# Kernel tuning notes

Measured on AMD Instinct MI355X. Metric: run time of the kernel, lower is better.

The kernel has to match this reference:

```python
import jax, jax.numpy as jnp
import numpy as np

BLOCK_SIZE = 128


def setup_inputs() -> dict:
    key = jax.random.key(0)
    kq, kk, kv = jax.random.split(key, 3)
    b, t, e = 16, 8192, 256
    Q = jax.random.normal(kq, (b, t, e), dtype=jnp.float32)
    K = jax.random.normal(kk, (b, t, e), dtype=jnp.float32)
    V = jax.random.normal(kv, (b, t, e), dtype=jnp.float32)
    return {"Q": Q, "K": K, "V": V}


def reference(Q, K, V):
    b, t, e = Q.shape
    bs = BLOCK_SIZE
    n = t // bs
    scale = 1.0 / jnp.sqrt(jnp.asarray(e, Q.dtype))
    Qb = Q.reshape(b, n, bs, e)
    Kb = K.reshape(b, n, bs, e)
    Vb = V.reshape(b, n, bs, e)
    # block-diagonal scores: [b, n, bs, bs]
    Z = jnp.einsum('bnqe,bnke->bnqk', Qb, Kb) * scale
    causal = jnp.triu(jnp.ones((bs, bs), dtype=bool), k=1)  # True above diagonal
    Z = jnp.where(causal, -jnp.inf, Z)
    A = jax.nn.softmax(Z, axis=-1)
    out = jnp.einsum('bnqk,bnke->bnqe', A, Vb).reshape(b, t, e)
    A_flat = A.reshape(b, t, bs)  # matches torch view(b, t, block_size)
    return out, A_flat
```

## Files before the change

kernel.cpp:

```cpp
#include <hip/hip_runtime.h>

#define T_  8192
#define E_  256
#define BS_ 128

typedef __attribute__((ext_vector_type(8))) short bf16x8;
typedef __attribute__((ext_vector_type(4))) float f32x4;

__device__ __forceinline__ unsigned short f2bf(float x) {
    unsigned int u = __float_as_uint(x);
    u += 0x7fffu + ((u >> 16) & 1u);
    return (unsigned short)(u >> 16);
}

__device__ __forceinline__ bf16x8 pack8(f32x4 a, f32x4 b) {
    bf16x8 r;
    r[0] = (short)f2bf(a[0]); r[1] = (short)f2bf(a[1]);
    r[2] = (short)f2bf(a[2]); r[3] = (short)f2bf(a[3]);
    r[4] = (short)f2bf(b[0]); r[5] = (short)f2bf(b[1]);
    r[6] = (short)f2bf(b[2]); r[7] = (short)f2bf(b[3]);
    return r;
}

__global__ __launch_bounds__(256, 2) void dba_qk_softmax(
        const float* __restrict__ Qg, const float* __restrict__ Kg,
        float* __restrict__ Ag)
{
    __shared__ unsigned short Ks[BS_ * E_];

    const int tid  = threadIdx.x;
    const int lane = tid & 63;
    const int w    = tid >> 6;
    const int cl   = lane & 15;
    const int g    = lane >> 4;
    const int bi   = blockIdx.x >> 6;
    const int ni   = blockIdx.x & 63;
    const int base  = (bi * T_ + ni * BS_) * E_;
    const int abase = (bi * T_ + ni * BS_) * BS_;

    {
        const int kq   = (tid & 63) * 4;
        const int nhi  = tid >> 6;
        const int chnk = kq >> 3;
        const int klow = kq & 7;
        #pragma unroll 8
        for (int i = 0; i < 32; ++i) {
            const int n = i * 4 + nhi;
            f32x4 kv = *(const f32x4*)(Kg + base + n * E_ + kq);
            const int chunkp = chnk ^ (n & 15);
            uint2 pk;
            pk.x = (unsigned)f2bf(kv[0]) | ((unsigned)f2bf(kv[1]) << 16);
            pk.y = (unsigned)f2bf(kv[2]) | ((unsigned)f2bf(kv[3]) << 16);
            *(uint2*)&Ks[n * E_ + chunkp * 8 + klow] = pk;
        }
    }
    __syncthreads();

    f32x4 acc[2][8];
    #pragma unroll
    for (int rt = 0; rt < 2; ++rt)
        #pragma unroll
        for (int nt = 0; nt < 8; ++nt)
            acc[rt][nt] = (f32x4){0.f, 0.f, 0.f, 0.f};

    const float* q0p = Qg + base + (w * 32 + cl) * E_;
    const float* q1p = q0p + 16 * E_;
    f32x4 q00 = *(const f32x4*)(q0p + g * 8);
    f32x4 q01 = *(const f32x4*)(q0p + g * 8 + 4);
    f32x4 q10 = *(const f32x4*)(q1p + g * 8);
    f32x4 q11 = *(const f32x4*)(q1p + g * 8 + 4);

    for (int ks = 0; ks < 8; ++ks) {
        bf16x8 aq0 = pack8(q00, q01);
        bf16x8 aq1 = pack8(q10, q11);
        if (ks < 7) {
            const int kn = (ks + 1) * 32 + g * 8;
            q00 = *(const f32x4*)(q0p + kn);
            q01 = *(const f32x4*)(q0p + kn + 4);
            q10 = *(const f32x4*)(q1p + kn);
            q11 = *(const f32x4*)(q1p + kn + 4);
        }
        const int chunkp = (ks * 4 + g) ^ cl;
        #pragma unroll
        for (int nt = 0; nt < 8; ++nt) {
            const int n = nt * 16 + cl;
            bf16x8 bk = *(const bf16x8*)&Ks[n * E_ + chunkp * 8];
            acc[0][nt] = __builtin_amdgcn_mfma_f32_16x16x32_bf16(aq0, bk, acc[0][nt], 0, 0, 0);
            acc[1][nt] = __builtin_amdgcn_mfma_f32_16x16x32_bf16(aq1, bk, acc[1][nt], 0, 0, 0);
        }
    }

    const float scale = 0.0625f;
    const float L2E   = 1.4426950408889634f;
    #pragma unroll
    for (int rt = 0; rt < 2; ++rt) {
        #pragma unroll
        for (int r = 0; r < 4; ++r) {
            const int q = w * 32 + rt * 16 + g * 4 + r;
            float m = -__builtin_inff();
            #pragma unroll
            for (int nt = 0; nt < 8; ++nt) {
                const int c = nt * 16 + cl;
                float z = acc[rt][nt][r] * scale;
                z = (c > q) ? -__builtin_inff() : z;
                acc[rt][nt][r] = z;
                m = fmaxf(m, z);
            }
            m = fmaxf(m, __shfl_xor(m, 1));
            m = fmaxf(m, __shfl_xor(m, 2));
            m = fmaxf(m, __shfl_xor(m, 4));
            m = fmaxf(m, __shfl_xor(m, 8));
            float s = 0.f;
            #pragma unroll
            for (int nt = 0; nt < 8; ++nt) {
                const float p = exp2f((acc[rt][nt][r] - m) * L2E);
                acc[rt][nt][r] = p;
                s += p;
            }
            s += __shfl_xor(s, 1);
            s += __shfl_xor(s, 2);
            s += __shfl_xor(s, 4);
            s += __shfl_xor(s, 8);
            const float rinv = __builtin_amdgcn_rcpf(s);
            #pragma unroll
            for (int nt = 0; nt < 8; ++nt)
                acc[rt][nt][r] *= rinv;
        }
    }

    #pragma unroll
    for (int rt = 0; rt < 2; ++rt)
        #pragma unroll
        for (int nt = 0; nt < 8; ++nt)
            #pragma unroll
            for (int r = 0; r < 4; ++r)
                Ag[abase + (w * 32 + rt * 16 + g * 4 + r) * BS_ + nt * 16 + cl] = acc[rt][nt][r];
}

__global__ __launch_bounds__(256, 2) void dba_av(
        const float* __restrict__ Ag, const float* __restrict__ Vg,
        float* __restrict__ Og)
{
    __shared__ unsigned short Vs[E_ * BS_];

    const int tid  = threadIdx.x;
    const int lane = tid & 63;
    const int w    = tid >> 6;
    const int cl   = lane & 15;
    const int g    = lane >> 4;
    const int bi   = blockIdx.x >> 6;
    const int ni   = blockIdx.x & 63;
    const int base  = (bi * T_ + ni * BS_) * E_;
    const int abase = (bi * T_ + ni * BS_) * BS_;

    {
        const int n  = tid;
        const int nx = n & 15;
        #pragma unroll 8
        for (int i = 0; i < 32; ++i) {
            const int k = i * 4;
            const float* vp = Vg + base + k * E_ + n;
            const float v0 = vp[0];
            const float v1 = vp[E_];
            const float v2 = vp[2 * E_];
            const float v3 = vp[3 * E_];
            const int chunkp = (k >> 3) ^ nx;
            uint2 pk;
            pk.x = (unsigned)f2bf(v0) | ((unsigned)f2bf(v1) << 16);
            pk.y = (unsigned)f2bf(v2) | ((unsigned)f2bf(v3) << 16);
            *(uint2*)&Vs[n * BS_ + chunkp * 8 + (k & 7)] = pk;
        }
    }
    __syncthreads();

    f32x4 acc[2][16];
    #pragma unroll
    for (int rt = 0; rt < 2; ++rt)
        #pragma unroll
        for (int nt = 0; nt < 16; ++nt)
            acc[rt][nt] = (f32x4){0.f, 0.f, 0.f, 0.f};

    const float* a0p = Ag + abase + (w * 32 + cl) * BS_;
    const float* a1p = a0p + 16 * BS_;
    f32x4 a00 = *(const f32x4*)(a0p + g * 8);
    f32x4 a01 = *(const f32x4*)(a0p + g * 8 + 4);
    f32x4 a10 = *(const f32x4*)(a1p + g * 8);
    f32x4 a11 = *(const f32x4*)(a1p + g * 8 + 4);

    for (int ks = 0; ks < 4; ++ks) {
        bf16x8 fa0 = pack8(a00, a01);
        bf16x8 fa1 = pack8(a10, a11);
        if (ks < 3) {
            const int kn = (ks + 1) * 32 + g * 8;
            a00 = *(const f32x4*)(a0p + kn);
            a01 = *(const f32x4*)(a0p + kn + 4);
            a10 = *(const f32x4*)(a1p + kn);
            a11 = *(const f32x4*)(a1p + kn + 4);
        }
        const int chunkp = (ks * 4 + g) ^ cl;
        #pragma unroll
        for (int nt = 0; nt < 16; ++nt) {
            const int nn = nt * 16 + cl;
            bf16x8 bv = *(const bf16x8*)&Vs[nn * BS_ + chunkp * 8];
            acc[0][nt] = __builtin_amdgcn_mfma_f32_16x16x32_bf16(fa0, bv, acc[0][nt], 0, 0, 0);
            acc[1][nt] = __builtin_amdgcn_mfma_f32_16x16x32_bf16(fa1, bv, acc[1][nt], 0, 0, 0);
        }
    }

    #pragma unroll
    for (int rt = 0; rt < 2; ++rt)
        #pragma unroll
        for (int nt = 0; nt < 16; ++nt)
            #pragma unroll
            for (int r = 0; r < 4; ++r)
                Og[base + (w * 32 + rt * 16 + g * 4 + r) * E_ + nt * 16 + cl] = acc[rt][nt][r];
}

extern "C" void kernel_launch(void* const* d_in, const int* in_sizes, int n_in,
                              void* d_out, int out_size, void* d_ws, size_t ws_size,
                              hipStream_t stream) {
    const float* Q = (const float*)d_in[0];
    const float* K = (const float*)d_in[1];
    const float* V = (const float*)d_in[2];
    float* O = (float*)d_out;
    const int b = in_sizes[0] / (T_ * E_);
    float* A = O + (size_t)b * T_ * E_;
    dim3 grid(b * (T_ / BS_));
    dim3 block(256);
    dba_qk_softmax<<<grid, block, 0, stream>>>(Q, K, A);
    dba_av<<<grid, block, 0, stream>>>(A, V, O);
}
```

Before: 474.9 us.

## Fuse QK-softmax and AV into one kernel reusing shared memory

Merges the two kernels into a single 512-thread kernel. Each block first stages K in shared memory and computes the softmaxed scores, writes A to global, then reloads V into the same shared buffer and reads its own A rows back to compute the output. Each wave now handles 16 query rows instead of 32, and Q/K/V loads and O stores use nontemporal hints. The intent is to drop the second launch and let the A read-back come from cache instead of HBM. The cost is an extra block barrier and halved per-wave MFMA reuse of the B-operand fragments read from shared memory.

```diff
diff --git a/kernel.cpp b/kernel.cpp
--- a/kernel.cpp
+++ b/kernel.cpp
@@ -22,11 +22,12 @@
     return r;
 }
 
-__global__ __launch_bounds__(256, 2) void dba_qk_softmax(
+__global__ __launch_bounds__(512, 4) void dba_fused(
         const float* __restrict__ Qg, const float* __restrict__ Kg,
-        float* __restrict__ Ag)
+        const float* __restrict__ Vg, float* __restrict__ Ag,
+        float* __restrict__ Og)
 {
-    __shared__ unsigned short Ks[BS_ * E_];
+    __shared__ unsigned short Sm[BS_ * E_];
 
     const int tid  = threadIdx.x;
     const int lane = tid & 63;
@@ -39,181 +40,140 @@
     const int abase = (bi * T_ + ni * BS_) * BS_;
 
     {
-        const int kq   = (tid & 63) * 4;
-        const int nhi  = tid >> 6;
-        const int chnk = kq >> 3;
-        const int klow = kq & 7;
-        #pragma unroll 8
-        for (int i = 0; i < 32; ++i) {
-            const int n = i * 4 + nhi;
-            f32x4 kv = *(const f32x4*)(Kg + base + n * E_ + kq);
-            const int chunkp = chnk ^ (n & 15);
+        const int c4   = lane * 4;
+        const int chnk = c4 >> 3;
+        const int klow = c4 & 7;
+        #pragma unroll 4
+        for (int i = 0; i < 16; ++i) {
+            const int n = i * 8 + w;
+            f32x4 kv = __builtin_nontemporal_load((const f32x4*)(Kg + base + n * E_ + c4));
+            const int cp = chnk ^ (n & 15);
             uint2 pk;
             pk.x = (unsigned)f2bf(kv[0]) | ((unsigned)f2bf(kv[1]) << 16);
             pk.y = (unsigned)f2bf(kv[2]) | ((unsigned)f2bf(kv[3]) << 16);
-            *(uint2*)&Ks[n * E_ + chunkp * 8 + klow] = pk;
+            *(uint2*)&Sm[n * E_ + cp * 8 + klow] = pk;
         }
     }
     __syncthreads();
 
-    f32x4 acc[2][8];
+    f32x4 acc[8];
     #pragma unroll
-    for (int rt = 0; rt < 2; ++rt)
-        #pragma unroll
-        for (int nt = 0; nt < 8; ++nt)
-            acc[rt][nt] = (f32x4){0.f, 0.f, 0.f, 0.f};
+    for (int nt = 0; nt < 8; ++nt) acc[nt] = (f32x4){0.f, 0.f, 0.f, 0.f};
 
-    const float* q0p = Qg + base + (w * 32 + cl) * E_;
-    const float* q1p = q0p + 16 * E_;
-    f32x4 q00 = *(const f32x4*)(q0p + g * 8);
-    f32x4 q01 = *(const f32x4*)(q0p + g * 8 + 4);
-    f32x4 q10 = *(const f32x4*)(q1p + g * 8);
-    f32x4 q11 = *(const f32x4*)(q1p + g * 8 + 4);
+    const float* qp = Qg + base + (w * 16 + cl) * E_;
+    f32x4 q0 = __builtin_nontemporal_load((const f32x4*)(qp + g * 8));
+    f32x4 q1 = __builtin_nontemporal_load((const f32x4*)(qp + g * 8 + 4));
 
     for (int ks = 0; ks < 8; ++ks) {
-        bf16x8 aq0 = pack8(q00, q01);
-        bf16x8 aq1 = pack8(q10, q11);
+        bf16x8 aq = pack8(q0, q1);
         if (ks < 7) {
             const int kn = (ks + 1) * 32 + g * 8;
-            q00 = *(const f32x4*)(q0p + kn);
-            q01 = *(const f32x4*)(q0p + kn + 4);
-            q10 = *(const f32x4*)(q1p + kn);
-            q11 = *(const f32x4*)(q1p + kn + 4);
+            q0 = __builtin_nontemporal_load((const f32x4*)(qp + kn));
+            q1 = __builtin_nontemporal_load((const f32x4*)(qp + kn + 4));
         }
-        const int chunkp = (ks * 4 + g) ^ cl;
         #pragma unroll
         for (int nt = 0; nt < 8; ++nt) {
-            const int n = nt * 16 + cl;
-            bf16x8 bk = *(const bf16x8*)&Ks[n * E_ + chunkp * 8];
-            acc[0][nt] = __builtin_amdgcn_mfma_f32_16x16x32_bf16(aq0, bk, acc[0][nt], 0, 0, 0);
-            acc[1][nt] = __builtin_amdgcn_mfma_f32_16x16x32_bf16(aq1, bk, acc[1][nt], 0, 0, 0);
+            const int n  = nt * 16 + cl;
+            const int cp = (ks * 4 + g) ^ cl;
+            bf16x8 bk = *(const bf16x8*)&Sm[n * E_ + cp * 8];
+            acc[nt] = __builtin_amdgcn_mfma_f32_16x16x32_bf16(aq, bk, acc[nt], 0, 0, 0);
         }
     }
 
     const float scale = 0.0625f;
     const float L2E   = 1.4426950408889634f;
     #pragma unroll
-    for (int rt = 0; rt < 2; ++rt) {
+    for (int r = 0; r < 4; ++r) {
+        const int q = w * 16 + g * 4 + r;
+        float m = -__builtin_inff();
         #pragma unroll
-        for (int r = 0; r < 4; ++r) {
-            const int q = w * 32 + rt * 16 + g * 4 + r;
-            float m = -__builtin_inff();
-            #pragma unroll
-            for (int nt = 0; nt < 8; ++nt) {
-                const int c = nt * 16 + cl;
-                float z = acc[rt][nt][r] * scale;
-                z = (c > q) ? -__builtin_inff() : z;
-                acc[rt][nt][r] = z;
-                m = fmaxf(m, z);
-            }
-            m = fmaxf(m, __shfl_xor(m, 1));
-            m = fmaxf(m, __shfl_xor(m, 2));
-            m = fmaxf(m, __shfl_xor(m, 4));
-            m = fmaxf(m, __shfl_xor(m, 8));
-            float s = 0.f;
-            #pragma unroll
-            for (int nt = 0; nt < 8; ++nt) {
-                const float p = exp2f((acc[rt][nt][r] - m) * L2E);
-                acc[rt][nt][r] = p;
-                s += p;
-            }
-            s += __shfl_xor(s, 1);
-            s += __shfl_xor(s, 2);
-            s += __shfl_xor(s, 4);
-            s += __shfl_xor(s, 8);
-            const float rinv = __builtin_amdgcn_rcpf(s);
-            #pragma unroll
-            for (int nt = 0; nt < 8; ++nt)
-                acc[rt][nt][r] *= rinv;
+        for (int nt = 0; nt < 8; ++nt) {
+            const int c = nt * 16 + cl;
+            float z = acc[nt][r] * scale;
+            z = (c > q) ? -__builtin_inff() : z;
+            acc[nt][r] = z;
+            m = fmaxf(m, z);
+        }
+        m = fmaxf(m, __shfl_xor(m, 1));
+        m = fmaxf(m, __shfl_xor(m, 2));
+        m = fmaxf(m, __shfl_xor(m, 4));
+        m = fmaxf(m, __shfl_xor(m, 8));
+        float s = 0.f;
+        #pragma unroll
+        for (int nt = 0; nt < 8; ++nt) {
+            const float p = exp2f((acc[nt][r] - m) * L2E);
+            acc[nt][r] = p;
+            s += p;
+        }
+        s += __shfl_xor(s, 1);
+        s += __shfl_xor(s, 2);
+        s += __shfl_xor(s, 4);
+        s += __shfl_xor(s, 8);
+        const float rinv = __builtin_amdgcn_rcpf(s);
+        #pragma unroll
+        for (int nt = 0; nt < 8; ++nt)
+            acc[nt][r] *= rinv;
+    }
+
+    #pragma unroll
+    for (int nt = 0; nt < 8; ++nt)
+        #pragma unroll
+        for (int r = 0; r < 4; ++r)
+            Ag[abase + (w * 16 + g * 4 + r) * BS_ + nt * 16 + cl] = acc[nt][r];
+
+    __syncthreads();
+
+    {
+        const int n  = tid & 255;
+        const int kh = (tid >> 8) * 64;
+        const int nx = n & 15;
+        #pragma unroll 4
+        for (int i = 0; i < 16; ++i) {
+            const int k = kh + i * 4;
+            const float* vp = Vg + base + k * E_ + n;
+            const float v0 = __builtin_nontemporal_load(vp);
+            const float v1 = __builtin_nontemporal_load(vp + E_);
+            const float v2 = __builtin_nontemporal_load(vp + 2 * E_);
+            const float v3 = __builtin_nontemporal_load(vp + 3 * E_);
+            const int cp = (k >> 3) ^ nx;
+            uint2 pk;
+            pk.x = (unsigned)f2bf(v0) | ((unsigned)f2bf(v1) << 16);
+            pk.y = (unsigned)f2bf(v2) | ((unsigned)f2bf(v3) << 16);
+            *(uint2*)&Sm[n * BS_ + cp * 8 + (k & 7)] = pk;
+        }
+    }
+    __syncthreads();
+
+    f32x4 acc2[16];
+    #pragma unroll
+    for (int nt = 0; nt < 16; ++nt) acc2[nt] = (f32x4){0.f, 0.f, 0.f, 0.f};
+
+    const float* ap = Ag + abase + (w * 16 + cl) * BS_;
+    f32x4 a0 = *(const f32x4*)(ap + g * 8);
+    f32x4 a1 = *(const f32x4*)(ap + g * 8 + 4);
+
+    for (int ks = 0; ks < 4; ++ks) {
+        bf16x8 fa = pack8(a0, a1);
+        if (ks < 3) {
+            const int kn = (ks + 1) * 32 + g * 8;
+            a0 = *(const f32x4*)(ap + kn);
+            a1 = *(const f32x4*)(ap + kn + 4);
+        }
+        #pragma unroll
+        for (int nt = 0; nt < 16; ++nt) {
+            const int nn = nt * 16 + cl;
+            const int cp = (ks * 4 + g) ^ cl;
+            bf16x8 bv = *(const bf16x8*)&Sm[nn * BS_ + cp * 8];
+            acc2[nt] = __builtin_amdgcn_mfma_f32_16x16x32_bf16(fa, bv, acc2[nt], 0, 0, 0);
         }
     }
 
     #pragma unroll
-    for (int rt = 0; rt < 2; ++rt)
+    for (int nt = 0; nt < 16; ++nt)
         #pragma unroll
-        for (int nt = 0; nt < 8; ++nt)
-            #pragma unroll
-            for (int r = 0; r < 4; ++r)
-                Ag[abase + (w * 32 + rt * 16 + g * 4 + r) * BS_ + nt * 16 + cl] = acc[rt][nt][r];
-}
-
-__global__ __launch_bounds__(256, 2) void dba_av(
-        const float* __restrict__ Ag, const float* __restrict__ Vg,
-        float* __restrict__ Og)
-{
-    __shared__ unsigned short Vs[E_ * BS_];
-
-    const int tid  = threadIdx.x;
-    const int lane = tid & 63;
-    const int w    = tid >> 6;
-    const int cl   = lane & 15;
-    const int g    = lane >> 4;
-    const int bi   = blockIdx.x >> 6;
-    const int ni   = blockIdx.x & 63;
-    const int base  = (bi * T_ + ni * BS_) * E_;
-    const int abase = (bi * T_ + ni * BS_) * BS_;
-
-    {
-        const int n  = tid;
-        const int nx = n & 15;
-        #pragma unroll 8
-        for (int i = 0; i < 32; ++i) {
-            const int k = i * 4;
-            const float* vp = Vg + base + k * E_ + n;
-            const float v0 = vp[0];
-            const float v1 = vp[E_];
-            const float v2 = vp[2 * E_];
-            const float v3 = vp[3 * E_];
-            const int chunkp = (k >> 3) ^ nx;
-            uint2 pk;
-            pk.x = (unsigned)f2bf(v0) | ((unsigned)f2bf(v1) << 16);
-            pk.y = (unsigned)f2bf(v2) | ((unsigned)f2bf(v3) << 16);
-            *(uint2*)&Vs[n * BS_ + chunkp * 8 + (k & 7)] = pk;
-        }
-    }
-    __syncthreads();
-
-    f32x4 acc[2][16];
-    #pragma unroll
-    for (int rt = 0; rt < 2; ++rt)
-        #pragma unroll
-        for (int nt = 0; nt < 16; ++nt)
-            acc[rt][nt] = (f32x4){0.f, 0.f, 0.f, 0.f};
-
-    const float* a0p = Ag + abase + (w * 32 + cl) * BS_;
-    const float* a1p = a0p + 16 * BS_;
-    f32x4 a00 = *(const f32x4*)(a0p + g * 8);
-    f32x4 a01 = *(const f32x4*)(a0p + g * 8 + 4);
-    f32x4 a10 = *(const f32x4*)(a1p + g * 8);
-    f32x4 a11 = *(const f32x4*)(a1p + g * 8 + 4);
-
-    for (int ks = 0; ks < 4; ++ks) {
-        bf16x8 fa0 = pack8(a00, a01);
-        bf16x8 fa1 = pack8(a10, a11);
-        if (ks < 3) {
-            const int kn = (ks + 1) * 32 + g * 8;
-            a00 = *(const f32x4*)(a0p + kn);
-            a01 = *(const f32x4*)(a0p + kn + 4);
-            a10 = *(const f32x4*)(a1p + kn);
-            a11 = *(const f32x4*)(a1p + kn + 4);
-        }
-        const int chunkp = (ks * 4 + g) ^ cl;
-        #pragma unroll
-        for (int nt = 0; nt < 16; ++nt) {
-            const int nn = nt * 16 + cl;
-            bf16x8 bv = *(const bf16x8*)&Vs[nn * BS_ + chunkp * 8];
-            acc[0][nt] = __builtin_amdgcn_mfma_f32_16x16x32_bf16(fa0, bv, acc[0][nt], 0, 0, 0);
-            acc[1][nt] = __builtin_amdgcn_mfma_f32_16x16x32_bf16(fa1, bv, acc[1][nt], 0, 0, 0);
-        }
-    }
-
-    #pragma unroll
-    for (int rt = 0; rt < 2; ++rt)
-        #pragma unroll
-        for (int nt = 0; nt < 16; ++nt)
-            #pragma unroll
-            for (int r = 0; r < 4; ++r)
-                Og[base + (w * 32 + rt * 16 + g * 4 + r) * E_ + nt * 16 + cl] = acc[rt][nt][r];
+        for (int r = 0; r < 4; ++r)
+            __builtin_nontemporal_store(acc2[nt][r],
+                Og + base + (w * 16 + g * 4 + r) * E_ + nt * 16 + cl);
 }
 
 extern "C" void kernel_launch(void* const* d_in, const int* in_sizes, int n_in,
@@ -226,7 +186,6 @@
     const int b = in_sizes[0] / (T_ * E_);
     float* A = O + (size_t)b * T_ * E_;
     dim3 grid(b * (T_ / BS_));
-    dim3 block(256);
-    dba_qk_softmax<<<grid, block, 0, stream>>>(Q, K, A);
-    dba_av<<<grid, block, 0, stream>>>(A, V, O);
+    dim3 block(512);
+    dba_fused<<<grid, block, 0, stream>>>(Q, K, V, A, O);
 }
```

After: 439.5 us. 1.08x faster.
